# Optimization experiments

Measured on AMD Instinct MI355X. Metric: run time of the kernel, lower is better.

## Reference

```python
import jax, jax.numpy as jnp
import numpy as np
import math

B, C, T = 4, 512, 2048
LN_EPS = 1e-5

def setup_inputs() -> dict:
    key = jax.random.key(0)
    ks = jax.random.split(key, 12)
    s = 1.0 / math.sqrt(C)
    inp = {
        'feat': jax.random.normal(ks[0], (B, C, T), dtype=jnp.float32),
        'Wq': jax.random.normal(ks[1], (C, C), dtype=jnp.float32) * s,
        'bq': jax.random.normal(ks[2], (C,), dtype=jnp.float32) * s,
        'Wk': jax.random.normal(ks[3], (C, C), dtype=jnp.float32) * s,
        'bk': jax.random.normal(ks[4], (C,), dtype=jnp.float32) * s,
        'Wv': jax.random.normal(ks[5], (C, C), dtype=jnp.float32) * s,
        'bv': jax.random.normal(ks[6], (C,), dtype=jnp.float32) * s,
        'Ws': jax.random.normal(ks[7], (C, C), dtype=jnp.float32) * s,
        'bs': jax.random.normal(ks[8], (C,), dtype=jnp.float32) * s,
        'Wl': jax.random.normal(ks[9], (C,), dtype=jnp.float32) * s,
        'bl': jax.random.normal(ks[10], (1,), dtype=jnp.float32) * s,
    }
    return inp

def reference(feat, Wq, bq, Wk, bk, Wv, bv, Ws, bs, Wl, bl):
    d = feat.shape[1]
    # 1x1 Conv1d == per-position linear over channels. feat: [B,C,T]
    value = jnp.einsum('oc,bct->bto', Wv, feat) + bv          # [B,T,C]
    query = jnp.einsum('oc,bct->bto', Wq, feat) + bq          # [B,T,C]
    key_  = jnp.einsum('oc,bct->bct', Wk, feat) + bk[:, None] # [B,C,T]
    f = jnp.einsum('btc,bcs->bts', query, key_) / math.sqrt(d)
    f = jax.nn.softmax(f, axis=2)                             # [B,T,T]
    y = jnp.einsum('bts,bsc->btc', f, value)                  # [B,T,C]
    f_score = jax.nn.sigmoid(jnp.einsum('btc,c->bt', y, Wl) + bl[0])
    z = jnp.einsum('bts,bsc->btc', 1.0 - f, value)            # [B,T,C]
    b_score = 1.0 - jax.nn.sigmoid(jnp.einsum('btc,c->bt', z, Wl) + bl[0])
    f_score = (f_score + b_score) / 2.0
    y_ct = jnp.einsum('oc,btc->bot', Ws, y) + bs[:, None]     # smooth conv, [B,C,T]
    out = feat + y_ct
    # LayerNorm over (C, T) jointly, default affine (weight=1, bias=0)
    mu = jnp.mean(out, axis=(1, 2), keepdims=True)
    var = jnp.mean(jnp.square(out - mu), axis=(1, 2), keepdims=True)
    out = (out - mu) * jax.lax.rsqrt(var + LN_EPS)
    return out, f_score
```

## Files before the change

kernel.cpp:

```cpp
#include <hip/hip_runtime.h>
#include <hip/hip_bf16.h>

#define BB 4
#define CC 512
#define TT 2048
static constexpr long CT  = (long)CC * TT;
static constexpr long TC  = (long)TT * CC;
static constexpr long TTT = (long)TT * TT;
static constexpr float SM_SCALE = 0.04419417382415922f;

typedef __bf16 bf16;
typedef __attribute__((ext_vector_type(8))) __bf16 bf16x8;
typedef __attribute__((ext_vector_type(4))) __bf16 bf16x4;
typedef __attribute__((ext_vector_type(4))) float f32x4;

__device__ __forceinline__ void load_lds16(const bf16* g, bf16* l)
{
    __builtin_amdgcn_global_load_lds(
        (const __attribute__((address_space(1))) void*)g,
        (__attribute__((address_space(3))) void*)l, 16, 0, 0);
}

#define FENCE asm volatile("" ::: "memory")

template <int TM, int TN, int WR, int WC, int BK>
struct CorePipe {
    static constexpr int THREADS = WR * WC * 64;
    static constexpr int MI = TM / (WR * 16);
    static constexpr int NI = TN / (WC * 16);
    static constexpr int CPR = BK / 8;
    static constexpr int RSH = (BK == 64) ? 3 : 2;
    static constexpr int CMASK = CPR - 1;
    static constexpr int CHUNKS = (TM + TN) * CPR;
    static constexpr int ACH = TM * CPR;
    static constexpr int CPT = CHUNKS / THREADS;
    static_assert(CPT * THREADS == CHUNKS, "chunk divisibility");
    static_assert(CPT == 4, "vmcnt literals below assume 4 loads/thread/tile");

    __device__ static __forceinline__ void stage(
        const bf16* __restrict__ Ab, const bf16* __restrict__ Bb,
        int K, int m0, int n0, int t, int p, bf16* As, bf16* Bs, int tid)
    {
#pragma unroll
        for (int i = 0; i < CPT; ++i) {
            int c = tid + i * THREADS;
            if (c < ACH) {
                int row = c >> RSH;
                int gc  = (c & CMASK) ^ (row & CMASK);
                load_lds16(Ab + (long)(m0 + row) * K + t * BK + gc * 8,
                           As + p * (TM * BK) + c * 8);
            } else {
                int d = c - ACH;
                int row = d >> RSH;
                int gc  = (d & CMASK) ^ (row & CMASK);
                load_lds16(Bb + (long)(n0 + row) * K + t * BK + gc * 8,
                           Bs + p * (TN * BK) + d * 8);
            }
        }
    }

    __device__ static __forceinline__ void run(
        const bf16* __restrict__ Ab, const bf16* __restrict__ Bb,
        int K, int m0, int n0, bf16* As, bf16* Bs, f32x4 (&acc)[MI][NI])
    {
        const int tid  = threadIdx.x;
        const int lane = tid & 63;
        const int wid  = tid >> 6;
        const int wr = (wid / WC) * (MI * 16);
        const int wc = (wid % WC) * (NI * 16);
        const int lm = lane & 15;
        const int lq = lane >> 4;
        const int nt = K / BK;

        stage(Ab, Bb, K, m0, n0, 0, 0, As, Bs, tid);
        stage(Ab, Bb, K, m0, n0, 1, 1, As, Bs, tid);
        asm volatile("s_waitcnt vmcnt(4)" ::: "memory");
        FENCE; __builtin_amdgcn_s_barrier(); FENCE;

        for (int t = 0; t < nt; ++t) {
            const int p = t & 1;
            const bf16* Ap = As + p * (TM * BK);
            const bf16* Bp = Bs + p * (TN * BK);
            bf16x8 af[BK / 32][MI], bfr[BK / 32][NI];
#pragma unroll
            for (int ks = 0; ks < BK / 32; ++ks) {
#pragma unroll
                for (int i = 0; i < MI; ++i) {
                    int ar = wr + i * 16 + lm;
                    int cc = (ks * 4 + lq) ^ (ar & CMASK);
                    af[ks][i] = *(const bf16x8*)(Ap + ar * BK + cc * 8);
                }
#pragma unroll
                for (int i = 0; i < NI; ++i) {
                    int br = wc + i * 16 + lm;
                    int cc = (ks * 4 + lq) ^ (br & CMASK);
                    bfr[ks][i] = *(const bf16x8*)(Bp + br * BK + cc * 8);
                }
            }
            asm volatile("s_waitcnt lgkmcnt(0)" ::: "memory");
            __builtin_amdgcn_sched_barrier(0);
            FENCE; __builtin_amdgcn_s_barrier(); FENCE;
            if (t + 2 < nt)
                stage(Ab, Bb, K, m0, n0, t + 2, p, As, Bs, tid);
            __builtin_amdgcn_s_setprio(1);
#pragma unroll
            for (int ks = 0; ks < BK / 32; ++ks)
#pragma unroll
                for (int mi = 0; mi < MI; ++mi)
#pragma unroll
                    for (int ni = 0; ni < NI; ++ni)
                        acc[mi][ni] = __builtin_amdgcn_mfma_f32_16x16x32_bf16(
                            af[ks][mi], bfr[ks][ni], acc[mi][ni], 0, 0, 0);
            __builtin_amdgcn_s_setprio(0);
            if (t + 1 < nt) {
                if (t + 2 < nt)
                    asm volatile("s_waitcnt vmcnt(4)" ::: "memory");
                else
                    asm volatile("s_waitcnt vmcnt(0)" ::: "memory");
                FENCE; __builtin_amdgcn_s_barrier(); FENCE;
            }
        }
    }
};

using CP = CorePipe<128, 128, 4, 2, 64>;

struct CoreQVPipe {
    static constexpr int THREADS = 512;
    static constexpr int MI = 2;
    static constexpr int NI = 4;
    static constexpr int BK = 64;
    static constexpr int CPR = 8, RSH = 3, CMASK = 7;
    static constexpr int ACH = 128 * 8;
    static constexpr int CHUNKS = 256 * 8;
    static constexpr int CPT = CHUNKS / THREADS;

    __device__ static __forceinline__ void stage(
        const bf16* __restrict__ Ab, const bf16* __restrict__ Bq,
        const bf16* __restrict__ Bv, int m0, int t, int p,
        bf16* As, bf16* Bs, int tid)
    {
#pragma unroll
        for (int i = 0; i < CPT; ++i) {
            int c = tid + i * THREADS;
            if (c < ACH) {
                int row = c >> RSH;
                int gc  = (c & CMASK) ^ (row & CMASK);
                load_lds16(Ab + (long)(m0 + row) * 512 + t * 64 + gc * 8,
                           As + p * (128 * 64) + c * 8);
            } else {
                int d = c - ACH;
                int row = d >> RSH;
                int gc  = (d & CMASK) ^ (row & CMASK);
                const bf16* src = (row < 64)
                    ? Bq + (long)row * 512
                    : Bv + (long)(row - 64) * 512;
                load_lds16(src + t * 64 + gc * 8, Bs + p * (128 * 64) + d * 8);
            }
        }
    }

    __device__ static __forceinline__ void run(
        const bf16* __restrict__ Ab, const bf16* __restrict__ Bq,
        const bf16* __restrict__ Bv,
        int m0, bf16* As, bf16* Bs, f32x4 (&acc)[MI][NI])
    {
        const int tid  = threadIdx.x;
        const int lane = tid & 63;
        const int wid  = tid >> 6;
        const int wr = (wid / 2) * 32;
        const int wc = (wid % 2) * 64;
        const int lm = lane & 15;
        const int lq = lane >> 4;
        const int nt = 8;

        stage(Ab, Bq, Bv, m0, 0, 0, As, Bs, tid);
        stage(Ab, Bq, Bv, m0, 1, 1, As, Bs, tid);
        asm volatile("s_waitcnt vmcnt(4)" ::: "memory");
        FENCE; __builtin_amdgcn_s_barrier(); FENCE;

        for (int t = 0; t < nt; ++t) {
            const int p = t & 1;
            const bf16* Ap = As + p * (128 * 64);
            const bf16* Bp = Bs + p * (128 * 64);
            bf16x8 af[2][MI], bfr[2][NI];
#pragma unroll
            for (int ks = 0; ks < 2; ++ks) {
#pragma unroll
                for (int i = 0; i < MI; ++i) {
                    int ar = wr + i * 16 + lm;
                    int cc = (ks * 4 + lq) ^ (ar & CMASK);
                    af[ks][i] = *(const bf16x8*)(Ap + ar * BK + cc * 8);
                }
#pragma unroll
                for (int i = 0; i < NI; ++i) {
                    int br = wc + i * 16 + lm;
                    int cc = (ks * 4 + lq) ^ (br & CMASK);
                    bfr[ks][i] = *(const bf16x8*)(Bp + br * BK + cc * 8);
                }
            }
            asm volatile("s_waitcnt lgkmcnt(0)" ::: "memory");
            __builtin_amdgcn_sched_barrier(0);
            FENCE; __builtin_amdgcn_s_barrier(); FENCE;
            if (t + 2 < nt)
                stage(Ab, Bq, Bv, m0, t + 2, p, As, Bs, tid);
            __builtin_amdgcn_s_setprio(1);
#pragma unroll
            for (int ks = 0; ks < 2; ++ks)
#pragma unroll
                for (int mi = 0; mi < MI; ++mi)
#pragma unroll
                    for (int ni = 0; ni < NI; ++ni)
                        acc[mi][ni] = __builtin_amdgcn_mfma_f32_16x16x32_bf16(
                            af[ks][mi], bfr[ks][ni], acc[mi][ni], 0, 0, 0);
            __builtin_amdgcn_s_setprio(0);
            if (t + 1 < nt) {
                if (t + 2 < nt)
                    asm volatile("s_waitcnt vmcnt(4)" ::: "memory");
                else
                    asm volatile("s_waitcnt vmcnt(0)" ::: "memory");
                FENCE; __builtin_amdgcn_s_barrier(); FENCE;
            }
        }
    }
};

__global__ __launch_bounds__(512)
void gemm_qv_kernel(const bf16* __restrict__ featT, const bf16* __restrict__ Wq_bf,
                    const bf16* __restrict__ Wv_bf, bf16* __restrict__ Qb,
                    bf16* __restrict__ Vn, const float* __restrict__ bq,
                    const float* __restrict__ bv, const float* __restrict__ wkc,
                    const float* __restrict__ bk, float* __restrict__ qb,
                    const float* __restrict__ Wl, float* __restrict__ vl)
{
    __shared__ __align__(16) bf16 As[2 * 128 * 64];
    __shared__ __align__(16) bf16 Bs[2 * 128 * 64];
    const int rb = blockIdx.z;
    const int m0 = blockIdx.y * 128;
    const int ng = blockIdx.x;
    const long wofs = (long)(ng * 64) * 512;
    f32x4 acc[2][4] = {};
    CoreQVPipe::run(featT + (long)rb * TC, Wq_bf + wofs, Wv_bf + wofs, m0, As, Bs, acc);

    const int lane = threadIdx.x & 63, wid = threadIdx.x >> 6;
    const int wr = (wid / 2) * 32;
    const bool isV = wid & 1;
    const int lm = lane & 15, lq = lane >> 4;

    if (isV) {
        bf16* outV = Vn + (long)rb * TC;
        float* vlb = vl + (long)rb * TT;
        float vs_[2][4] = {};
#pragma unroll
        for (int mi = 0; mi < 2; ++mi)
#pragma unroll
            for (int ni = 0; ni < 4; ++ni) {
                int n = ng * 64 + ni * 16 + lm;
                float bn = bv[n], wn = Wl[n];
#pragma unroll
                for (int r = 0; r < 4; ++r) {
                    int m = m0 + wr + mi * 16 + lq * 4 + r;
                    float v = acc[mi][ni][r] + bn;
                    outV[(long)m * 512 + n] = (bf16)v;
                    vs_[mi][r] += v * wn;
                }
            }
#pragma unroll
        for (int mi = 0; mi < 2; ++mi)
#pragma unroll
            for (int r = 0; r < 4; ++r) {
                float s = vs_[mi][r];
                s += __shfl_xor(s, 1, 64); s += __shfl_xor(s, 2, 64);
                s += __shfl_xor(s, 4, 64); s += __shfl_xor(s, 8, 64);
                if (lm == 0)
                    atomicAdd(vlb + m0 + wr + mi * 16 + lq * 4 + r, s);
            }
    } else {
        bf16* out = Qb + (long)rb * TC;
        float* qbb = qb + (long)rb * TT;
        float rs[2][4] = {};
#pragma unroll
        for (int mi = 0; mi < 2; ++mi)
#pragma unroll
            for (int ni = 0; ni < 4; ++ni) {
                int n = ng * 64 + ni * 16 + lm;
                float bn = bq[n], wn = wkc[n], kn = bk[n];
#pragma unroll
                for (int r = 0; r < 4; ++r) {
                    int m = m0 + wr + mi * 16 + lq * 4 + r;
                    float v = acc[mi][ni][r] + bn;
                    rs[mi][r] += v * kn;
                    out[(long)m * 512 + n] = (bf16)(v * wn);
                }
            }
#pragma unroll
        for (int mi = 0; mi < 2; ++mi)
#pragma unroll
            for (int r = 0; r < 4; ++r) {
                float s = rs[mi][r];
                s += __shfl_xor(s, 1, 64); s += __shfl_xor(s, 2, 64);
                s += __shfl_xor(s, 4, 64); s += __shfl_xor(s, 8, 64);
                if (lm == 0)
                    atomicAdd(qbb + m0 + wr + mi * 16 + lq * 4 + r, s);
            }
    }
}

__global__ __launch_bounds__(512, 2)
void gemm_s256_kernel(const bf16* __restrict__ Qb, const bf16* __restrict__ featT,
                      bf16* __restrict__ S, const float* __restrict__ qb,
                      float* __restrict__ rsum, const float* __restrict__ vl,
                      float* __restrict__ u)
{
    __shared__ __align__(16) bf16 lds[2][2][256 * 64];
    const int id   = blockIdx.x;
    const int xcd  = id & 7, sIdx = id >> 3;
    const int bz   = xcd >> 1;
    const int n0   = (sIdx & 7) * 256;
    const int m0   = (((xcd & 1) << 2) + (sIdx >> 3)) * 256;
    const bf16* __restrict__ Ab = Qb + (long)bz * TC;
    const bf16* __restrict__ Bb = featT + (long)bz * TC;

    const int tid  = threadIdx.x;
    const int lane = tid & 63;
    const int wid  = tid >> 6;
    const int lm = lane & 15, lq = lane >> 4;
    const int wrb = (wid >> 2) * 64;
    const int wcb = (wid & 3) * 32;

    f32x4 acc[8][4] = {};

#define STAGE_HT(t, op, h)                                                    \
    do {                                                                      \
        const bf16* gp_ = (op) ? Bb : Ab;                                     \
        const int  br_  = ((op) ? n0 : m0) + (h) * 128;                       \
        bf16* lp_ = &lds[(t) & 1][op][(h) * 128 * 64];                        \
        _Pragma("unroll")                                                     \
        for (int i_ = 0; i_ < 2; ++i_) {                                      \
            int c_ = tid + i_ * 512;                                          \
            int r_ = c_ >> 3;                                                 \
            int g_ = (c_ & 7) ^ (r_ & 7);                                     \
            load_lds16(gp_ + (long)(br_ + r_) * 512 + (t) * 64 + g_ * 8,      \
                       lp_ + c_ * 8);                                         \
        }                                                                     \
    } while (0)

#define PHASE(t, qm, qn, doSt, st, sop, sh, doVm)                             \
    do {                                                                      \
        bf16x8 af[2][4], bfr[2][2];                                           \
        const bf16* Al_ = lds[(t) & 1][0];                                    \
        const bf16* Bl_ = lds[(t) & 1][1];                                    \
        _Pragma("unroll")                                                     \
        for (int ks = 0; ks < 2; ++ks) {                                      \
            _Pragma("unroll")                                                 \
            for (int j = 0; j < 4; ++j) {                                     \
                int ar = (qm) * 128 + wrb + j * 16 + lm;                      \
                int cc = (ks * 4 + lq) ^ (ar & 7);                            \
                af[ks][j] = *(const bf16x8*)(Al_ + ar * 64 + cc * 8);         \
            }                                                                 \
            _Pragma("unroll")                                                 \
            for (int j = 0; j < 2; ++j) {                                     \
                int br = (qn) * 128 + wcb + j * 16 + lm;                      \
                int cc = (ks * 4 + lq) ^ (br & 7);                            \
                bfr[ks][j] = *(const bf16x8*)(Bl_ + br * 64 + cc * 8);        \
            }                                                                 \
        }                                                                     \
        if (doSt) STAGE_HT(st, sop, sh);                                      \
        if (doVm) {                                                           \
            if ((t) < 6) asm volatile("s_waitcnt vmcnt(4)" ::: "memory");     \
            else         asm volatile("s_waitcnt vmcnt(0)" ::: "memory");     \
        }                                                                     \
        FENCE; __builtin_amdgcn_s_barrier(); FENCE;                           \
        __builtin_amdgcn_s_setprio(1);                                        \
        _Pragma("unroll")                                                     \
        for (int ks = 0; ks < 2; ++ks)                                        \
            _Pragma("unroll")                                                 \
            for (int j = 0; j < 4; ++j)                                       \
                _Pragma("unroll")                                             \
                for (int j2 = 0; j2 < 2; ++j2)                                \
                    acc[(qm) * 4 + j][(qn) * 2 + j2] =                        \
                        __builtin_amdgcn_mfma_f32_16x16x32_bf16(              \
                            af[ks][j], bfr[ks][j2],                           \
                            acc[(qm) * 4 + j][(qn) * 2 + j2], 0, 0, 0);       \
        __builtin_amdgcn_s_setprio(0);                                        \
        FENCE; __builtin_amdgcn_s_barrier(); FENCE;                           \
    } while (0)

    STAGE_HT(0, 0, 0); STAGE_HT(0, 1, 0); STAGE_HT(0, 0, 1); STAGE_HT(0, 1, 1);
    STAGE_HT(1, 0, 0); STAGE_HT(1, 1, 0);
    asm volatile("s_waitcnt vmcnt(4)" ::: "memory");
    FENCE; __builtin_amdgcn_s_barrier(); FENCE;

    for (int t = 0; t < 8; ++t) {
        PHASE(t, 0, 0, t + 1 < 8, t + 1, 0, 1, false);
        PHASE(t, 0, 1, t + 1 < 8, t + 1, 1, 1, false);
        PHASE(t, 1, 0, t + 2 < 8, t + 2, 0, 0, false);
        PHASE(t, 1, 1, t + 2 < 8, t + 2, 1, 0, true);
    }
#undef PHASE
#undef STAGE_HT

    bf16* outp = S + (long)bz * TTT;
    const float* qbb = qb + (long)bz * TT;
    const float* vlb = vl + (long)bz * TT;
    float* rsb = rsum + (long)bz * TT;
    float* ub  = u + (long)bz * TT;
#pragma unroll
    for (int mi = 0; mi < 8; ++mi) {
        const int mrow = m0 + (mi >> 2) * 128 + wrb + (mi & 3) * 16 + lq * 4;
        const f32x4 qv = *(const f32x4*)(qbb + mrow);
        float rp[4] = {0.f, 0.f, 0.f, 0.f};
        float up[4] = {0.f, 0.f, 0.f, 0.f};
#pragma unroll
        for (int ni = 0; ni < 4; ++ni) {
            const int ncol = n0 + (ni >> 1) * 128 + wcb + (ni & 1) * 16 + lm;
            const float vlv = vlb[ncol];
#pragma unroll
            for (int r = 0; r < 4; ++r) {
                float p = __expf((acc[mi][ni][r] + qv[r]) * SM_SCALE);
                outp[(long)(mrow + r) * 2048 + ncol] = (bf16)p;
                rp[r] += p;
                up[r] += p * vlv;
            }
        }
#pragma unroll
        for (int r = 0; r < 4; ++r) {
            float s2 = rp[r], s3 = up[r];
            s2 += __shfl_xor(s2, 1, 64); s2 += __shfl_xor(s2, 2, 64);
            s2 += __shfl_xor(s2, 4, 64); s2 += __shfl_xor(s2, 8, 64);
            s3 += __shfl_xor(s3, 1, 64); s3 += __shfl_xor(s3, 2, 64);
            s3 += __shfl_xor(s3, 4, 64); s3 += __shfl_xor(s3, 8, 64);
            if (lm == 0) {
                atomicAdd(rsb + mrow + r, s2);
                atomicAdd(ub + mrow + r, s3);
            }
        }
    }
}

__global__ __launch_bounds__(512)
void gemm_vs_kernel(const bf16* __restrict__ Vn, const bf16* __restrict__ Ws_bf,
                    bf16* __restrict__ Vpt)
{
    __shared__ __align__(16) bf16 As[2 * 128 * 64];
    __shared__ __align__(16) bf16 Bs[2 * 128 * 64];
    const int id = blockIdx.x;
    const int xcd = id & 7, s = id >> 3;
    const int bz = xcd >> 1;
    const int m0 = (((xcd & 1) << 1) + (s >> 4)) * 128;
    const int n0 = (s & 15) * 128;
    f32x4 acc[2][4] = {};
    CP::run(Ws_bf, Vn + (long)bz * TC, 512, m0, n0, As, Bs, acc);

    const int lane = threadIdx.x & 63, wid = threadIdx.x >> 6;
    const int wr = (wid / 2) * 32, wc = (wid % 2) * 64;
    const int lm = lane & 15, lq = lane >> 4;
    bf16* out = Vpt + (long)bz * CT;
#pragma unroll
    for (int mi = 0; mi < 2; ++mi)
#pragma unroll
        for (int ni = 0; ni < 4; ++ni) {
            int n = n0 + wc + ni * 16 + lm;
#pragma unroll
            for (int r = 0; r < 4; ++r) {
                int m = m0 + wr + mi * 16 + lq * 4 + r;
                out[(long)m * 2048 + n] = (bf16)acc[mi][ni][r];
            }
        }
}

__global__ __launch_bounds__(512)
void gemm_out_kernel(const bf16* __restrict__ S, const bf16* __restrict__ Vpt,
                     float* __restrict__ out, const float* __restrict__ bs,
                     const float* __restrict__ feat,
                     const float* __restrict__ rsum, double* __restrict__ stats)
{
    __shared__ __align__(16) bf16 As[2 * 128 * 64];
    __shared__ __align__(16) bf16 Bs[2 * 128 * 64];
    __shared__ float red[16];
    const int id = blockIdx.x;
    const int xcd = id & 7, s = id >> 3;
    const int bz = xcd >> 1;
    const int n0 = (s & 3) * 128;
    const int m0 = (((xcd & 1) << 3) + (s >> 2)) * 128;
    f32x4 acc[2][4] = {};
    CP::run(S + (long)bz * TTT, Vpt + (long)bz * CT, 2048, m0, n0, As, Bs, acc);

    const int tid = threadIdx.x;
    const int lane = tid & 63, wid = tid >> 6;
    const int wr = (wid / 2) * 32, wc = (wid % 2) * 64;
    const int lm = lane & 15, lq = lane >> 4;
    const float* rsb = rsum + (long)bz * TT;
    float inv[2][4];
#pragma unroll
    for (int mi = 0; mi < 2; ++mi) {
        int mrow = m0 + wr + mi * 16 + lq * 4;
        f32x4 rv = *(const f32x4*)(rsb + mrow);
#pragma unroll
        for (int r = 0; r < 4; ++r) inv[mi][r] = 1.f / rv[r];
    }
    float s1 = 0.f, s2 = 0.f;
#pragma unroll
    for (int mi = 0; mi < 2; ++mi)
#pragma unroll
        for (int ni = 0; ni < 4; ++ni) {
            int mrow = m0 + wr + mi * 16 + lq * 4;
            int n = n0 + wc + ni * 16 + lm;
            long off = (long)bz * CT + (long)n * TT + mrow;
            f32x4 fv = *(const f32x4*)(feat + off);
            float bn = bs[n];
            f32x4 res;
#pragma unroll
            for (int r = 0; r < 4; ++r) {
                float v = acc[mi][ni][r] * inv[mi][r] + bn + fv[r];
                res[r] = v;
                s1 += v;
                s2 += v * v;
            }
            *(f32x4*)(out + off) = res;
        }
#pragma unroll
    for (int off = 32; off; off >>= 1) {
        s1 += __shfl_xor(s1, off, 64);
        s2 += __shfl_xor(s2, off, 64);
    }
    if (lane == 0) { red[wid] = s1; red[8 + wid] = s2; }
    __syncthreads();
    if (tid == 0) {
        double t1 = 0.0, t2 = 0.0;
#pragma unroll
        for (int w = 0; w < 8; ++w) { t1 += red[w]; t2 += red[8 + w]; }
        atomicAdd(stats + bz * 2, t1);
        atomicAdd(stats + bz * 2 + 1, t2);
    }
}

__global__ __launch_bounds__(256)
void prep_kernel(const float* __restrict__ feat, bf16* __restrict__ featT,
                 const float* __restrict__ Wq, const float* __restrict__ Wv,
                 const float* __restrict__ Ws, bf16* __restrict__ Wbf,
                 const float* __restrict__ Wk, const float* __restrict__ Wl,
                 const float* __restrict__ bv, float* __restrict__ wkc,
                 float* __restrict__ wvl, float* __restrict__ wlbv,
                 float* __restrict__ frp, float* __restrict__ qb,
                 float* __restrict__ u, float* __restrict__ rsum,
                 double* __restrict__ stats, float* __restrict__ vl)
{
    const int blk = blockIdx.x;
    const int tid = threadIdx.x;
    if (blk < 4096) {
        __shared__ float tile[32][33];
        __shared__ float sfr[4][32];
        const int b  = blk >> 10;
        const int c0 = ((blk & 1023) >> 6) * 32;
        const int tt = blk & 63;
        const int t0 = tt * 32;
        const int tx = tid & 31;
        const int ty = tid >> 5;
#pragma unroll
        for (int j = 0; j < 4; ++j) {
            int c = c0 + ty + j * 8;
            tile[ty + j * 8][tx] = feat[(long)b * CT + (long)c * TT + t0 + tx];
        }
        __syncthreads();
        float ps = 0.f;
#pragma unroll
        for (int j = 0; j < 4; ++j) {
            int tl = ty + j * 8;
            int t = t0 + tl;
            int c = c0 + tx;
            float v = tile[tx][tl];
            ps += v;
            featT[(long)b * TC + (long)t * CC + c] = (bf16)v;
        }
        const int wid = tid >> 6;
        ps += __shfl_xor(ps, 32, 64);
        if ((tid & 63) < 32) sfr[wid][tx] = ps;
        __syncthreads();
        if (tid < 32) {
            float s = sfr[0][tid] + sfr[1][tid] + sfr[2][tid] + sfr[3][tid];
            frp[(((long)b * 64 + tt) << 9) + c0 + tid] = s;
        }
    } else if (blk < 4480) {
        long gid = (long)(blk - 4096) * 256 + tid;
        long idx = gid * 8;
        int w = (int)(idx >> 18);
        long off = idx & 262143;
        const float* src = (w == 0) ? Wq : (w == 1) ? Wv : Ws;
        f32x4 a = *(const f32x4*)(src + off);
        f32x4 b = *(const f32x4*)(src + off + 4);
        bf16x8 o;
#pragma unroll
        for (int j = 0; j < 4; ++j) { o[j] = (bf16)a[j]; o[4 + j] = (bf16)b[j]; }
        *(bf16x8*)(Wbf + idx) = o;
    } else {
        int mid = (blk - 4480) * 256 + tid;
        if (mid < 512) {
            float s = 0.f;
            for (int o = 0; o < 512; ++o) s += Wk[o * 512 + mid];
            wkc[mid] = s;
        } else if (mid < 1024) {
            int k = mid - 512;
            float s = 0.f;
            for (int c = 0; c < 512; ++c) s += Wl[c] * Wv[c * 512 + k];
            wvl[k] = s;
        } else if (mid < 1088) {
            int lane = mid - 1024;
            float s = 0.f;
#pragma unroll
            for (int j = 0; j < 8; ++j) s += Wl[lane + 64 * j] * bv[lane + 64 * j];
#pragma unroll
            for (int off = 32; off; off >>= 1) s += __shfl_xor(s, off, 64);
            if (lane == 0) wlbv[0] = s;
        } else if (mid >= 1152 && mid < 1160) {
            stats[mid - 1152] = 0.0;
        } else if (mid >= 4096 && mid < 12288) {
            qb[mid - 4096] = 0.f;
        } else if (mid >= 12288 && mid < 20480) {
            u[mid - 12288] = 0.f;
        } else if (mid >= 20480 && mid < 28672) {
            rsum[mid - 20480] = 0.f;
        } else if (mid >= 28672 && mid < 36864) {
            vl[mid - 28672] = 0.f;
        }
    }
}

__global__ __launch_bounds__(256)
void ln_score_kernel(float* __restrict__ out, const double* __restrict__ stats,
                     const float* __restrict__ u, const float* __restrict__ frp,
                     const float* __restrict__ wvl, const float* __restrict__ wlbv,
                     const float* __restrict__ blp, const float* __restrict__ rsum)
{
    if (blockIdx.x < 4096) {
        long i = ((long)blockIdx.x * 256 + threadIdx.x) * 4;
        int b = (int)(i >> 20);
        const double n = 1048576.0;
        double mu  = stats[b * 2] / n;
        double var = stats[b * 2 + 1] / n - mu * mu;
        float rs = (float)(1.0 / sqrt(var + 1e-5));
        float muf = (float)mu;
        f32x4 v = *(f32x4*)(out + i);
#pragma unroll
        for (int j = 0; j < 4; ++j) v[j] = (v[j] - muf) * rs;
        *(f32x4*)(out + i) = v;
    } else {
        const int b = blockIdx.x - 4096;
        __shared__ float ssv[4];
        const int tid = threadIdx.x, lane = tid & 63, wid = tid >> 6;
        const float* fb = frp + ((long)b * 64 << 9);
        float s0 = 0.f, s1 = 0.f;
#pragma unroll 8
        for (int k = 0; k < 64; ++k) {
            s0 += fb[(k << 9) + tid];
            s1 += fb[(k << 9) + tid + 256];
        }
        float p = s0 * wvl[tid] + s1 * wvl[tid + 256];
#pragma unroll
        for (int off = 32; off; off >>= 1) p += __shfl_xor(p, off, 64);
        if (lane == 0) ssv[wid] = p;
        __syncthreads();
        const float sv = ssv[0] + ssv[1] + ssv[2] + ssv[3] + 2048.f * wlbv[0];
        const float bl0 = blp[0];
#pragma unroll
        for (int j = 0; j < 8; ++j) {
            int t = tid + j * 256;
            float uu = u[(long)b * TT + t] / rsum[(long)b * TT + t];
            float uf = uu + bl0;
            float vf = sv - uu + bl0;
            float fs  = 1.f / (1.f + __expf(-uf));
            float bsc = 1.f - 1.f / (1.f + __expf(-vf));
            out[(long)BB * CT + (long)b * TT + t] = 0.5f * (fs + bsc);
        }
    }
}

extern "C" void kernel_launch(void* const* d_in, const int* in_sizes, int n_in,
                              void* d_out, int out_size, void* d_ws, size_t ws_size,
                              hipStream_t stream)
{
    const float* feat = (const float*)d_in[0];
    const float* Wq   = (const float*)d_in[1];
    const float* bq   = (const float*)d_in[2];
    const float* Wk   = (const float*)d_in[3];
    const float* bk   = (const float*)d_in[4];
    const float* Wv   = (const float*)d_in[5];
    const float* bv   = (const float*)d_in[6];
    const float* Ws   = (const float*)d_in[7];
    const float* bs   = (const float*)d_in[8];
    const float* Wl   = (const float*)d_in[9];
    const float* bl   = (const float*)d_in[10];
    float* out = (float*)d_out;

    if (ws_size < 69316736) return;
    char* ws = (char*)d_ws;
    bf16* featT  = (bf16*)(ws);
    bf16* Wbf    = (bf16*)(ws + 8388608);
    bf16* Qb     = (bf16*)(ws + 9961472);
    bf16* Vn     = (bf16*)(ws + 18350080);
    bf16* Vpt    = (bf16*)(ws + 26738688);
    float* vl    = (float*)(ws + 26738688);
    bf16* S      = (bf16*)(ws + 35127296);
    float* wkc   = (float*)(ws + 68689920);
    float* wvl   = (float*)(ws + 68691968);
    float* wlbv  = (float*)(ws + 68694016);
    float* qb    = (float*)(ws + 68694080);
    double* stats= (double*)(ws + 68726848);
    float* u     = (float*)(ws + 68726912);
    float* rsum  = (float*)(ws + 68759680);
    float* frp   = (float*)(ws + 68792448);

    bf16* Wq_bf = Wbf;
    bf16* Wv_bf = Wbf + 262144;
    bf16* Ws_bf = Wbf + 524288;

    prep_kernel<<<4624, 256, 0, stream>>>(feat, featT, Wq, Wv, Ws, Wbf, Wk, Wl, bv,
                                          wkc, wvl, wlbv, frp, qb, u, rsum, stats, vl);
    gemm_qv_kernel<<<dim3(8, 16, 4), 512, 0, stream>>>(
        featT, Wq_bf, Wv_bf, Qb, Vn, bq, bv, wkc, bk, qb, Wl, vl);
    gemm_s256_kernel<<<256, 512, 0, stream>>>(Qb, featT, S, qb, rsum, vl, u);
    gemm_vs_kernel<<<256, 512, 0, stream>>>(Vn, Ws_bf, Vpt);
    gemm_out_kernel<<<256, 512, 0, stream>>>(S, Vpt, out, bs, feat, rsum, stats);
    ln_score_kernel<<<4100, 256, 0, stream>>>(out, stats, u, frp, wvl, wlbv, bl, rsum);
}
```

Before: 211.7 us.

## Deepen GEMM pipeline to three stages and retile output GEMM to 64x256

Generalizes the shared GEMM core pipeline to a configurable prefetch depth and uses triple-buffered LDS for the Ws·V and S·V output GEMMs, so global loads have more time to land before they are consumed. The output GEMM also changes from 128x128 tiles with a 4x2 wave grid to 64x256 tiles with 1x8 waves, which spans the full C dimension in two tiles and reshapes reuse of the attention-score rows. This uses more LDS per block, which may lower occupancy, and changes the epilogue indexing.

After: 215.0 us. No clear change (+1.6%).

```diff
diff --git a/kernel.cpp b/kernel.cpp
--- a/kernel.cpp
+++ b/kernel.cpp
@@ -23,7 +23,18 @@
 
 #define FENCE asm volatile("" ::: "memory")
 
-template <int TM, int TN, int WR, int WC, int BK>
+template <int N> __device__ __forceinline__ void vm_wait()
+{
+    if constexpr (N == 0)       asm volatile("s_waitcnt vmcnt(0)" ::: "memory");
+    else if constexpr (N == 4)  asm volatile("s_waitcnt vmcnt(4)" ::: "memory");
+    else if constexpr (N == 5)  asm volatile("s_waitcnt vmcnt(5)" ::: "memory");
+    else if constexpr (N == 8)  asm volatile("s_waitcnt vmcnt(8)" ::: "memory");
+    else if constexpr (N == 10) asm volatile("s_waitcnt vmcnt(10)" ::: "memory");
+    else if constexpr (N == 12) asm volatile("s_waitcnt vmcnt(12)" ::: "memory");
+    else static_assert(N == 0, "unsupported vmcnt literal");
+}
+
+template <int TM, int TN, int WR, int WC, int BK, int DEPTH>
 struct CorePipe {
     static constexpr int THREADS = WR * WC * 64;
     static constexpr int MI = TM / (WR * 16);
@@ -35,7 +46,7 @@
     static constexpr int ACH = TM * CPR;
     static constexpr int CPT = CHUNKS / THREADS;
     static_assert(CPT * THREADS == CHUNKS, "chunk divisibility");
-    static_assert(CPT == 4, "vmcnt literals below assume 4 loads/thread/tile");
+    static_assert(DEPTH == 2 || DEPTH == 3, "depth 2 or 3");
 
     __device__ static __forceinline__ void stage(
         const bf16* __restrict__ Ab, const bf16* __restrict__ Bb,
@@ -72,13 +83,14 @@
         const int lq = lane >> 4;
         const int nt = K / BK;
 
-        stage(Ab, Bb, K, m0, n0, 0, 0, As, Bs, tid);
-        stage(Ab, Bb, K, m0, n0, 1, 1, As, Bs, tid);
-        asm volatile("s_waitcnt vmcnt(4)" ::: "memory");
+#pragma unroll
+        for (int d = 0; d < DEPTH; ++d)
+            stage(Ab, Bb, K, m0, n0, d, d, As, Bs, tid);
+        vm_wait<CPT * (DEPTH - 1)>();
         FENCE; __builtin_amdgcn_s_barrier(); FENCE;
 
+        int p = 0;
         for (int t = 0; t < nt; ++t) {
-            const int p = t & 1;
             const bf16* Ap = As + p * (TM * BK);
             const bf16* Bp = Bs + p * (TN * BK);
             bf16x8 af[BK / 32][MI], bfr[BK / 32][NI];
@@ -100,8 +112,8 @@
             asm volatile("s_waitcnt lgkmcnt(0)" ::: "memory");
             __builtin_amdgcn_sched_barrier(0);
             FENCE; __builtin_amdgcn_s_barrier(); FENCE;
-            if (t + 2 < nt)
-                stage(Ab, Bb, K, m0, n0, t + 2, p, As, Bs, tid);
+            if (t + DEPTH < nt)
+                stage(Ab, Bb, K, m0, n0, t + DEPTH, p, As, Bs, tid);
             __builtin_amdgcn_s_setprio(1);
 #pragma unroll
             for (int ks = 0; ks < BK / 32; ++ks)
@@ -113,17 +125,19 @@
                             af[ks][mi], bfr[ks][ni], acc[mi][ni], 0, 0, 0);
             __builtin_amdgcn_s_setprio(0);
             if (t + 1 < nt) {
-                if (t + 2 < nt)
-                    asm volatile("s_waitcnt vmcnt(4)" ::: "memory");
-                else
-                    asm volatile("s_waitcnt vmcnt(0)" ::: "memory");
+                const int rem = nt - t;
+                if (rem > DEPTH)                    vm_wait<CPT * (DEPTH - 1)>();
+                else if (DEPTH == 3 && rem == 3)    vm_wait<CPT>();
+                else                                vm_wait<0>();
                 FENCE; __builtin_amdgcn_s_barrier(); FENCE;
             }
+            p = (p + 1 == DEPTH) ? 0 : p + 1;
         }
     }
 };
 
-using CP = CorePipe<128, 128, 4, 2, 64>;
+using CPVS  = CorePipe<128, 128, 4, 2, 64, 3>;
+using CPOUT = CorePipe<64, 256, 1, 8, 64, 3>;
 
 struct CoreQVPipe {
     static constexpr int THREADS = 512;
@@ -176,7 +190,7 @@
 
         stage(Ab, Bq, Bv, m0, 0, 0, As, Bs, tid);
         stage(Ab, Bq, Bv, m0, 1, 1, As, Bs, tid);
-        asm volatile("s_waitcnt vmcnt(4)" ::: "memory");
+        vm_wait<4>();
         FENCE; __builtin_amdgcn_s_barrier(); FENCE;
 
         for (int t = 0; t < nt; ++t) {
@@ -215,10 +229,8 @@
                             af[ks][mi], bfr[ks][ni], acc[mi][ni], 0, 0, 0);
             __builtin_amdgcn_s_setprio(0);
             if (t + 1 < nt) {
-                if (t + 2 < nt)
-                    asm volatile("s_waitcnt vmcnt(4)" ::: "memory");
-                else
-                    asm volatile("s_waitcnt vmcnt(0)" ::: "memory");
+                if (t + 2 < nt) vm_wait<4>();
+                else            vm_wait<0>();
                 FENCE; __builtin_amdgcn_s_barrier(); FENCE;
             }
         }
@@ -442,15 +454,15 @@
 void gemm_vs_kernel(const bf16* __restrict__ Vn, const bf16* __restrict__ Ws_bf,
                     bf16* __restrict__ Vpt)
 {
-    __shared__ __align__(16) bf16 As[2 * 128 * 64];
-    __shared__ __align__(16) bf16 Bs[2 * 128 * 64];
+    __shared__ __align__(16) bf16 As[3 * 128 * 64];
+    __shared__ __align__(16) bf16 Bs[3 * 128 * 64];
     const int id = blockIdx.x;
     const int xcd = id & 7, s = id >> 3;
     const int bz = xcd >> 1;
     const int m0 = (((xcd & 1) << 1) + (s >> 4)) * 128;
     const int n0 = (s & 15) * 128;
     f32x4 acc[2][4] = {};
-    CP::run(Ws_bf, Vn + (long)bz * TC, 512, m0, n0, As, Bs, acc);
+    CPVS::run(Ws_bf, Vn + (long)bz * TC, 512, m0, n0, As, Bs, acc);
 
     const int lane = threadIdx.x & 63, wid = threadIdx.x >> 6;
     const int wr = (wid / 2) * 32, wc = (wid % 2) * 64;
@@ -475,37 +487,36 @@
                      const float* __restrict__ feat,
                      const float* __restrict__ rsum, double* __restrict__ stats)
 {
-    __shared__ __align__(16) bf16 As[2 * 128 * 64];
-    __shared__ __align__(16) bf16 Bs[2 * 128 * 64];
+    __shared__ __align__(16) bf16 As[3 * 64 * 64];
+    __shared__ __align__(16) bf16 Bs[3 * 256 * 64];
     __shared__ float red[16];
     const int id = blockIdx.x;
-    const int xcd = id & 7, s = id >> 3;
+    const int xcd = id & 7, sIdx = id >> 3;
     const int bz = xcd >> 1;
-    const int n0 = (s & 3) * 128;
-    const int m0 = (((xcd & 1) << 3) + (s >> 2)) * 128;
-    f32x4 acc[2][4] = {};
-    CP::run(S + (long)bz * TTT, Vpt + (long)bz * CT, 2048, m0, n0, As, Bs, acc);
+    const int n0 = (sIdx & 1) * 256;
+    const int m0 = (((xcd & 1) << 4) + (sIdx >> 1)) * 64;
+    f32x4 acc[4][2] = {};
+    CPOUT::run(S + (long)bz * TTT, Vpt + (long)bz * CT, 2048, m0, n0, As, Bs, acc);
 
     const int tid = threadIdx.x;
     const int lane = tid & 63, wid = tid >> 6;
-    const int wr = (wid / 2) * 32, wc = (wid % 2) * 64;
     const int lm = lane & 15, lq = lane >> 4;
     const float* rsb = rsum + (long)bz * TT;
-    float inv[2][4];
-#pragma unroll
-    for (int mi = 0; mi < 2; ++mi) {
-        int mrow = m0 + wr + mi * 16 + lq * 4;
+    float inv[4][4];
+#pragma unroll
+    for (int mi = 0; mi < 4; ++mi) {
+        int mrow = m0 + mi * 16 + lq * 4;
         f32x4 rv = *(const f32x4*)(rsb + mrow);
 #pragma unroll
         for (int r = 0; r < 4; ++r) inv[mi][r] = 1.f / rv[r];
     }
     float s1 = 0.f, s2 = 0.f;
 #pragma unroll
-    for (int mi = 0; mi < 2; ++mi)
-#pragma unroll
-        for (int ni = 0; ni < 4; ++ni) {
-            int mrow = m0 + wr + mi * 16 + lq * 4;
-            int n = n0 + wc + ni * 16 + lm;
+    for (int mi = 0; mi < 4; ++mi)
+#pragma unroll
+        for (int ni = 0; ni < 2; ++ni) {
+            int mrow = m0 + mi * 16 + lq * 4;
+            int n = n0 + wid * 32 + ni * 16 + lm;
             long off = (long)bz * CT + (long)n * TT + mrow;
             f32x4 fv = *(const f32x4*)(feat + off);
             float bn = bs[n];
```
